# Kernel tuning notes

Hardware: AMD Instinct MI355X
Metric: run time of the kernel (lower is better)

## Reference

```python
import jax, jax.numpy as jnp
import numpy as np

NUM_USERS = 100000
NUM_ITEMS = 50000
EMBED_DIM = 64
NUM_EDGES = 4000000


def setup_inputs() -> dict:
    key = jax.random.key(0)
    k1, k2, k3, k4, k5 = jax.random.split(key, 5)
    u_emb = jax.random.normal(k1, (NUM_USERS, EMBED_DIM), dtype=jnp.float32)
    i_emb = jax.random.normal(k2, (NUM_ITEMS, EMBED_DIM), dtype=jnp.float32)
    user_idx = jax.random.randint(k3, (NUM_EDGES,), 0, 50000, dtype=jnp.int64 if jax.config.jax_enable_x64 else jnp.int32)
    item_idx = jax.random.randint(k4, (NUM_EDGES,), 0, 50000, dtype=jnp.int64 if jax.config.jax_enable_x64 else jnp.int32)
    edge_index = jnp.stack([user_idx, item_idx], axis=0)  # [2, E]
    weights = jax.random.uniform(k5, (NUM_EDGES,), dtype=jnp.float32)
    return {"u_emb": u_emb, "i_emb": i_emb, "edge_index": edge_index, "weights": weights}


def reference(u_emb, i_emb, edge_index, weights):
    user_idx, item_idx = edge_index[0], edge_index[1]
    num_users, num_items = u_emb.shape[0], i_emb.shape[0]
    ones = jnp.ones_like(weights)
    user_deg = jnp.clip(jax.ops.segment_sum(ones, user_idx, num_segments=num_users), 1.0)
    item_deg = jnp.clip(jax.ops.segment_sum(ones, item_idx, num_segments=num_items), 1.0)
    # per-edge symmetric degree normalization: 1/(sqrt(du)*sqrt(di))
    norm = jax.lax.rsqrt(user_deg[user_idx] * item_deg[item_idx])
    edge_w = (weights * norm)[:, None]  # [E, 1]
    new_u_emb = jax.ops.segment_sum(i_emb[item_idx] * edge_w, user_idx, num_segments=num_users)
    new_i_emb = jax.ops.segment_sum(u_emb[user_idx] * edge_w, item_idx, num_segments=num_items)
    return (new_u_emb, new_i_emb)
```

## Files before the change

kernel.cpp:

```cpp
#include <hip/hip_runtime.h>
#include <hip/hip_fp16.h>


#define NUSERS 100000
#define NITEMS 50000
#define EDIM 64
#define NEDGES 4000000

__global__ void degree_kernel(const int* __restrict__ uidx,
                              const int* __restrict__ iidx,
                              int* __restrict__ udeg,
                              int* __restrict__ ideg) {
    int stride = gridDim.x * blockDim.x;
    for (int e = blockIdx.x * blockDim.x + threadIdx.x; e < NEDGES; e += stride) {
        atomicAdd(&udeg[uidx[e]], 1);
        atomicAdd(&ideg[iidx[e]], 1);
    }
}

__global__ void scan_kernel(const int* __restrict__ udeg,
                            const int* __restrict__ ideg,
                            int* __restrict__ u_off, int* __restrict__ i_off,
                            int* __restrict__ u_cur, int* __restrict__ i_cur) {
    __shared__ int partial[1024];
    const int* cnt; int n; int* off; int* cur;
    if (blockIdx.x == 0) { cnt = udeg; n = NUSERS; off = u_off; cur = u_cur; }
    else                 { cnt = ideg; n = NITEMS; off = i_off; cur = i_cur; }

    int tid = threadIdx.x;
    int chunk = (n + 1023) >> 10;
    int s = tid * chunk;
    int e = min(s + chunk, n);

    int sum = 0;
    for (int i = s; i < e; ++i) sum += cnt[i];
    partial[tid] = sum;
    __syncthreads();

    for (int d = 1; d < 1024; d <<= 1) {
        int v = partial[tid];
        int add = (tid >= d) ? partial[tid - d] : 0;
        __syncthreads();
        partial[tid] = v + add;
        __syncthreads();
    }

    int run = partial[tid] - sum;
    for (int i = s; i < e; ++i) {
        off[i] = run;
        cur[i] = run;
        run += cnt[i];
    }
}

__device__ __forceinline__ unsigned pack_rec(int src_idx, float ew) {
    return (unsigned)src_idx |
           ((unsigned)__half_as_ushort(__float2half(ew)) << 16);
}

__global__ void build_u_kernel(const int* __restrict__ uidx,
                               const int* __restrict__ iidx,
                               const float* __restrict__ w,
                               const int* __restrict__ udeg,
                               const int* __restrict__ ideg,
                               int* __restrict__ u_cur,
                               unsigned* __restrict__ u_edges) {
    int stride = gridDim.x * blockDim.x;
    for (int e = blockIdx.x * blockDim.x + threadIdx.x; e < NEDGES; e += stride) {
        int u  = uidx[e];
        int it = iidx[e];
        float ew = w[e] * rsqrtf((float)max(udeg[u], 1) * (float)max(ideg[it], 1));
        int p = atomicAdd(&u_cur[u], 1);
        u_edges[p] = pack_rec(it, ew);
    }
}

__global__ void build_i_kernel(const int* __restrict__ uidx,
                               const int* __restrict__ iidx,
                               const float* __restrict__ w,
                               const int* __restrict__ udeg,
                               const int* __restrict__ ideg,
                               int* __restrict__ i_cur,
                               unsigned* __restrict__ i_edges) {
    int stride = gridDim.x * blockDim.x;
    for (int e = blockIdx.x * blockDim.x + threadIdx.x; e < NEDGES; e += stride) {
        int u  = uidx[e];
        int it = iidx[e];
        float ew = w[e] * rsqrtf((float)max(udeg[u], 1) * (float)max(ideg[it], 1));
        int p = atomicAdd(&i_cur[it], 1);
        i_edges[p] = pack_rec(u, ew);
    }
}

__global__ void gather_kernel(const unsigned* __restrict__ u_edges,
                              const unsigned* __restrict__ i_edges,
                              const int* __restrict__ u_off,
                              const int* __restrict__ i_off,
                              const int* __restrict__ udeg,
                              const int* __restrict__ ideg,
                              const float* __restrict__ u_emb,
                              const float* __restrict__ i_emb,
                              float* __restrict__ out_u,
                              float* __restrict__ out_i) {
    int t = blockIdx.x * blockDim.x + threadIdx.x;
    int row  = t >> 4;
    int lane = t & 15;

    const unsigned* edges; const int* off; const int* deg;
    const float* src; float* out; int r;
    if (row < NUSERS) {
        edges = u_edges; off = u_off; deg = udeg; src = i_emb; out = out_u; r = row;
    } else if (row < NUSERS + NITEMS) {
        edges = i_edges; off = i_off; deg = ideg; src = u_emb; out = out_i; r = row - NUSERS;
    } else {
        return;
    }

    int s = off[r];
    int n = deg[r];
    float4 acc = make_float4(0.f, 0.f, 0.f, 0.f);
    for (int k = 0; k < n; ++k) {
        unsigned rec = edges[s + k];
        float ew = __half2float(__ushort_as_half((unsigned short)(rec >> 16)));
        const float4 v = *reinterpret_cast<const float4*>(
            src + (size_t)(rec & 0xFFFFu) * EDIM + lane * 4);
        acc.x += v.x * ew;
        acc.y += v.y * ew;
        acc.z += v.z * ew;
        acc.w += v.w * ew;
    }
    *reinterpret_cast<float4*>(out + (size_t)r * EDIM + lane * 4) = acc;
}

__global__ void fb_degree_kernel(const int* __restrict__ uidx,
                                 const int* __restrict__ iidx,
                                 float* __restrict__ udeg,
                                 float* __restrict__ ideg) {
    int stride = gridDim.x * blockDim.x;
    for (int e = blockIdx.x * blockDim.x + threadIdx.x; e < NEDGES; e += stride) {
        atomicAdd(&udeg[uidx[e]], 1.0f);
        atomicAdd(&ideg[iidx[e]], 1.0f);
    }
}

__global__ void fb_scatter_kernel(const float* __restrict__ u_emb,
                                  const float* __restrict__ i_emb,
                                  const int* __restrict__ uidx,
                                  const int* __restrict__ iidx,
                                  const float* __restrict__ w,
                                  const float* __restrict__ udeg,
                                  const float* __restrict__ ideg,
                                  float* __restrict__ out_u,
                                  float* __restrict__ out_i) {
    long long t = (long long)blockIdx.x * blockDim.x + threadIdx.x;
    int e    = (int)(t >> 4);
    int lane = (int)(t & 15);
    if (e >= NEDGES) return;
    int u  = uidx[e];
    int it = iidx[e];
    float ew = w[e] * rsqrtf(fmaxf(udeg[u], 1.0f) * fmaxf(ideg[it], 1.0f));
    const float4 iv = *reinterpret_cast<const float4*>(i_emb + (size_t)it * EDIM + lane * 4);
    const float4 uv = *reinterpret_cast<const float4*>(u_emb + (size_t)u  * EDIM + lane * 4);
    float* pu = out_u + (size_t)u  * EDIM + lane * 4;
    float* pi = out_i + (size_t)it * EDIM + lane * 4;
    atomicAdd(pu + 0, iv.x * ew); atomicAdd(pu + 1, iv.y * ew);
    atomicAdd(pu + 2, iv.z * ew); atomicAdd(pu + 3, iv.w * ew);
    atomicAdd(pi + 0, uv.x * ew); atomicAdd(pi + 1, uv.y * ew);
    atomicAdd(pi + 2, uv.z * ew); atomicAdd(pi + 3, uv.w * ew);
}

extern "C" void kernel_launch(void* const* d_in, const int* in_sizes, int n_in,
                              void* d_out, int out_size, void* d_ws, size_t ws_size,
                              hipStream_t stream) {
    const float* u_emb = (const float*)d_in[0];
    const float* i_emb = (const float*)d_in[1];
    const int*   eidx  = (const int*)d_in[2];
    const float* w     = (const float*)d_in[3];

    const int* uidx = eidx;
    const int* iidx = eidx + NEDGES;

    float* out_u = (float*)d_out;
    float* out_i = out_u + (size_t)NUSERS * EDIM;

    size_t need = (size_t)NEDGES * 4 * 2 + (size_t)(NUSERS + NITEMS) * 4 * 3;

    if (ws_size >= need) {
        char* p = (char*)d_ws;
        unsigned* u_edges = (unsigned*)p;          p += (size_t)NEDGES * 4;
        unsigned* i_edges = (unsigned*)p;          p += (size_t)NEDGES * 4;
        int* udeg = (int*)p;                       p += (size_t)NUSERS * 4;
        int* ideg = (int*)p;                       p += (size_t)NITEMS * 4;
        int* u_off = (int*)p;                      p += (size_t)NUSERS * 4;
        int* i_off = (int*)p;                      p += (size_t)NITEMS * 4;
        int* u_cur = (int*)p;                      p += (size_t)NUSERS * 4;
        int* i_cur = (int*)p;

        hipMemsetAsync(udeg, 0, (size_t)(NUSERS + NITEMS) * 4, stream);

        degree_kernel<<<2048, 256, 0, stream>>>(uidx, iidx, udeg, ideg);
        scan_kernel<<<2, 1024, 0, stream>>>(udeg, ideg, u_off, i_off, u_cur, i_cur);
        build_u_kernel<<<2048, 256, 0, stream>>>(uidx, iidx, w, udeg, ideg,
                                                 u_cur, u_edges);
        build_i_kernel<<<2048, 256, 0, stream>>>(uidx, iidx, w, udeg, ideg,
                                                 i_cur, i_edges);
        int rows = NUSERS + NITEMS;
        gather_kernel<<<(rows * 16 + 255) / 256, 256, 0, stream>>>(
            u_edges, i_edges, u_off, i_off, udeg, ideg, u_emb, i_emb, out_u, out_i);
    } else {
        float* udeg = (float*)d_ws;
        float* ideg = udeg + NUSERS;
        hipMemsetAsync(d_ws, 0, (size_t)(NUSERS + NITEMS) * sizeof(float), stream);
        hipMemsetAsync(d_out, 0, (size_t)out_size * sizeof(float), stream);
        fb_degree_kernel<<<2048, 256, 0, stream>>>(uidx, iidx, udeg, ideg);
        long long total_threads = (long long)NEDGES * 16;
        fb_scatter_kernel<<<(int)((total_threads + 255) / 256), 256, 0, stream>>>(
            u_emb, i_emb, uidx, iidx, w, udeg, ideg, out_u, out_i);
    }
}
```

Baseline: 1.310 ms.

## Replicate degree counters and CSR cursors to reduce atomic contention

Degree counting and CSR slot assignment now use NREP=8 replicated counter arrays chosen by block index. A totals kernel sums the replicas for normalization and the scan, and a cursor-init kernel gives each replica its own sub-range within each row's CSR segment. This is meant to spread same-address atomics across copies and cut contention on hot rows. It adds two small kernels, a larger memset and workspace, and needs more workspace, so it may fall back to the atomic scatter path if the buffer is too small.

```diff
diff --git a/kernel.cpp b/kernel.cpp
--- a/kernel.cpp
+++ b/kernel.cpp
@@ -6,26 +6,53 @@
 #define NITEMS 50000
 #define EDIM 64
 #define NEDGES 4000000
-
-__global__ void degree_kernel(const int* __restrict__ uidx,
-                              const int* __restrict__ iidx,
-                              int* __restrict__ udeg,
-                              int* __restrict__ ideg) {
-    int stride = gridDim.x * blockDim.x;
-    for (int e = blockIdx.x * blockDim.x + threadIdx.x; e < NEDGES; e += stride) {
-        atomicAdd(&udeg[uidx[e]], 1);
-        atomicAdd(&ideg[iidx[e]], 1);
-    }
-}
-
-__global__ void scan_kernel(const int* __restrict__ udeg,
-                            const int* __restrict__ ideg,
-                            int* __restrict__ u_off, int* __restrict__ i_off,
-                            int* __restrict__ u_cur, int* __restrict__ i_cur) {
+#define NREP 8
+#define BUILD_GRID 2048
+#define BUILD_BLK 256
+
+__global__ void degree_rep_kernel(const int* __restrict__ uidx,
+                                  const int* __restrict__ iidx,
+                                  int* __restrict__ udeg_rep,
+                                  int* __restrict__ ideg_rep) {
+    int r = blockIdx.x & (NREP - 1);
+    int* __restrict__ ud = udeg_rep + (size_t)r * NUSERS;
+    int* __restrict__ id = ideg_rep + (size_t)r * NITEMS;
+    int stride = gridDim.x * blockDim.x;
+    for (int e = blockIdx.x * blockDim.x + threadIdx.x; e < NEDGES; e += stride) {
+        atomicAdd(&ud[uidx[e]], 1);
+        atomicAdd(&id[iidx[e]], 1);
+    }
+}
+
+__global__ void totals_kernel(const int* __restrict__ udeg_rep,
+                              const int* __restrict__ ideg_rep,
+                              int* __restrict__ udeg_tot,
+                              int* __restrict__ ideg_tot) {
+    int stride = gridDim.x * blockDim.x;
+    for (int row = blockIdx.x * blockDim.x + threadIdx.x;
+         row < NUSERS + NITEMS; row += stride) {
+        if (row < NUSERS) {
+            int s = 0;
+            #pragma unroll
+            for (int r = 0; r < NREP; ++r) s += udeg_rep[(size_t)r * NUSERS + row];
+            udeg_tot[row] = s;
+        } else {
+            int rr = row - NUSERS;
+            int s = 0;
+            #pragma unroll
+            for (int r = 0; r < NREP; ++r) s += ideg_rep[(size_t)r * NITEMS + rr];
+            ideg_tot[rr] = s;
+        }
+    }
+}
+
+__global__ void scan_kernel(const int* __restrict__ udeg_tot,
+                            const int* __restrict__ ideg_tot,
+                            int* __restrict__ u_off, int* __restrict__ i_off) {
     __shared__ int partial[1024];
-    const int* cnt; int n; int* off; int* cur;
-    if (blockIdx.x == 0) { cnt = udeg; n = NUSERS; off = u_off; cur = u_cur; }
-    else                 { cnt = ideg; n = NITEMS; off = i_off; cur = i_cur; }
+    const int* cnt; int n; int* off;
+    if (blockIdx.x == 0) { cnt = udeg_tot; n = NUSERS; off = u_off; }
+    else                 { cnt = ideg_tot; n = NITEMS; off = i_off; }
 
     int tid = threadIdx.x;
     int chunk = (n + 1023) >> 10;
@@ -48,8 +75,35 @@
     int run = partial[tid] - sum;
     for (int i = s; i < e; ++i) {
         off[i] = run;
-        cur[i] = run;
         run += cnt[i];
+    }
+}
+
+__global__ void cur_init_kernel(const int* __restrict__ udeg_rep,
+                                const int* __restrict__ ideg_rep,
+                                const int* __restrict__ u_off,
+                                const int* __restrict__ i_off,
+                                int* __restrict__ u_cur_rep,
+                                int* __restrict__ i_cur_rep) {
+    int stride = gridDim.x * blockDim.x;
+    for (int row = blockIdx.x * blockDim.x + threadIdx.x;
+         row < NUSERS + NITEMS; row += stride) {
+        if (row < NUSERS) {
+            int base = u_off[row];
+            #pragma unroll
+            for (int r = 0; r < NREP; ++r) {
+                u_cur_rep[(size_t)r * NUSERS + row] = base;
+                base += udeg_rep[(size_t)r * NUSERS + row];
+            }
+        } else {
+            int rr = row - NUSERS;
+            int base = i_off[rr];
+            #pragma unroll
+            for (int r = 0; r < NREP; ++r) {
+                i_cur_rep[(size_t)r * NITEMS + rr] = base;
+                base += ideg_rep[(size_t)r * NITEMS + rr];
+            }
+        }
     }
 }
 
@@ -61,16 +115,19 @@
 __global__ void build_u_kernel(const int* __restrict__ uidx,
                                const int* __restrict__ iidx,
                                const float* __restrict__ w,
-                               const int* __restrict__ udeg,
-                               const int* __restrict__ ideg,
-                               int* __restrict__ u_cur,
+                               const int* __restrict__ udeg_tot,
+                               const int* __restrict__ ideg_tot,
+                               int* __restrict__ u_cur_rep,
                                unsigned* __restrict__ u_edges) {
+    int rep = blockIdx.x & (NREP - 1);
+    int* __restrict__ cur = u_cur_rep + (size_t)rep * NUSERS;
     int stride = gridDim.x * blockDim.x;
     for (int e = blockIdx.x * blockDim.x + threadIdx.x; e < NEDGES; e += stride) {
         int u  = uidx[e];
         int it = iidx[e];
-        float ew = w[e] * rsqrtf((float)max(udeg[u], 1) * (float)max(ideg[it], 1));
-        int p = atomicAdd(&u_cur[u], 1);
+        float ew = w[e] * rsqrtf((float)max(udeg_tot[u], 1) *
+                                 (float)max(ideg_tot[it], 1));
+        int p = atomicAdd(&cur[u], 1);
         u_edges[p] = pack_rec(it, ew);
     }
 }
@@ -78,16 +135,19 @@
 __global__ void build_i_kernel(const int* __restrict__ uidx,
                                const int* __restrict__ iidx,
                                const float* __restrict__ w,
-                               const int* __restrict__ udeg,
-                               const int* __restrict__ ideg,
-                               int* __restrict__ i_cur,
+                               const int* __restrict__ udeg_tot,
+                               const int* __restrict__ ideg_tot,
+                               int* __restrict__ i_cur_rep,
                                unsigned* __restrict__ i_edges) {
+    int rep = blockIdx.x & (NREP - 1);
+    int* __restrict__ cur = i_cur_rep + (size_t)rep * NITEMS;
     int stride = gridDim.x * blockDim.x;
     for (int e = blockIdx.x * blockDim.x + threadIdx.x; e < NEDGES; e += stride) {
         int u  = uidx[e];
         int it = iidx[e];
-        float ew = w[e] * rsqrtf((float)max(udeg[u], 1) * (float)max(ideg[it], 1));
-        int p = atomicAdd(&i_cur[it], 1);
+        float ew = w[e] * rsqrtf((float)max(udeg_tot[u], 1) *
+                                 (float)max(ideg_tot[it], 1));
+        int p = atomicAdd(&cur[it], 1);
         i_edges[p] = pack_rec(u, ew);
     }
 }
@@ -96,8 +156,8 @@
                               const unsigned* __restrict__ i_edges,
                               const int* __restrict__ u_off,
                               const int* __restrict__ i_off,
-                              const int* __restrict__ udeg,
-                              const int* __restrict__ ideg,
+                              const int* __restrict__ udeg_tot,
+                              const int* __restrict__ ideg_tot,
                               const float* __restrict__ u_emb,
                               const float* __restrict__ i_emb,
                               float* __restrict__ out_u,
@@ -109,9 +169,10 @@
     const unsigned* edges; const int* off; const int* deg;
     const float* src; float* out; int r;
     if (row < NUSERS) {
-        edges = u_edges; off = u_off; deg = udeg; src = i_emb; out = out_u; r = row;
+        edges = u_edges; off = u_off; deg = udeg_tot; src = i_emb; out = out_u; r = row;
     } else if (row < NUSERS + NITEMS) {
-        edges = i_edges; off = i_off; deg = ideg; src = u_emb; out = out_i; r = row - NUSERS;
+        edges = i_edges; off = i_off; deg = ideg_tot; src = u_emb; out = out_i;
+        r = row - NUSERS;
     } else {
         return;
     }
@@ -183,30 +244,45 @@
     float* out_u = (float*)d_out;
     float* out_i = out_u + (size_t)NUSERS * EDIM;
 
-    size_t need = (size_t)NEDGES * 4 * 2 + (size_t)(NUSERS + NITEMS) * 4 * 3;
+    size_t need = (size_t)NEDGES * 4 * 2
+                + (size_t)(NUSERS + NITEMS) * 4 * (2 * NREP + 2)
+                + (size_t)(NUSERS + NITEMS) * 4;
 
     if (ws_size >= need) {
         char* p = (char*)d_ws;
         unsigned* u_edges = (unsigned*)p;          p += (size_t)NEDGES * 4;
         unsigned* i_edges = (unsigned*)p;          p += (size_t)NEDGES * 4;
-        int* udeg = (int*)p;                       p += (size_t)NUSERS * 4;
-        int* ideg = (int*)p;                       p += (size_t)NITEMS * 4;
+        int* udeg_rep = (int*)p;                   p += (size_t)NREP * NUSERS * 4;
+        int* ideg_rep = (int*)p;                   p += (size_t)NREP * NITEMS * 4;
+        int* udeg_tot = (int*)p;                   p += (size_t)NUSERS * 4;
+        int* ideg_tot = (int*)p;                   p += (size_t)NITEMS * 4;
         int* u_off = (int*)p;                      p += (size_t)NUSERS * 4;
         int* i_off = (int*)p;                      p += (size_t)NITEMS * 4;
-        int* u_cur = (int*)p;                      p += (size_t)NUSERS * 4;
-        int* i_cur = (int*)p;
-
-        hipMemsetAsync(udeg, 0, (size_t)(NUSERS + NITEMS) * 4, stream);
-
-        degree_kernel<<<2048, 256, 0, stream>>>(uidx, iidx, udeg, ideg);
-        scan_kernel<<<2, 1024, 0, stream>>>(udeg, ideg, u_off, i_off, u_cur, i_cur);
-        build_u_kernel<<<2048, 256, 0, stream>>>(uidx, iidx, w, udeg, ideg,
-                                                 u_cur, u_edges);
-        build_i_kernel<<<2048, 256, 0, stream>>>(uidx, iidx, w, udeg, ideg,
-                                                 i_cur, i_edges);
+        int* u_cur_rep = (int*)p;                  p += (size_t)NREP * NUSERS * 4;
+        int* i_cur_rep = (int*)p;
+
+        hipMemsetAsync(udeg_rep, 0, (size_t)NREP * (NUSERS + NITEMS) * 4, stream);
+
+        degree_rep_kernel<<<BUILD_GRID, BUILD_BLK, 0, stream>>>(
+            uidx, iidx, udeg_rep, ideg_rep);
+
         int rows = NUSERS + NITEMS;
+        totals_kernel<<<(rows + 255) / 256, 256, 0, stream>>>(
+            udeg_rep, ideg_rep, udeg_tot, ideg_tot);
+
+        scan_kernel<<<2, 1024, 0, stream>>>(udeg_tot, ideg_tot, u_off, i_off);
+
+        cur_init_kernel<<<(rows + 255) / 256, 256, 0, stream>>>(
+            udeg_rep, ideg_rep, u_off, i_off, u_cur_rep, i_cur_rep);
+
+        build_u_kernel<<<BUILD_GRID, BUILD_BLK, 0, stream>>>(
+            uidx, iidx, w, udeg_tot, ideg_tot, u_cur_rep, u_edges);
+        build_i_kernel<<<BUILD_GRID, BUILD_BLK, 0, stream>>>(
+            uidx, iidx, w, udeg_tot, ideg_tot, i_cur_rep, i_edges);
+
         gather_kernel<<<(rows * 16 + 255) / 256, 256, 0, stream>>>(
-            u_edges, i_edges, u_off, i_off, udeg, ideg, u_emb, i_emb, out_u, out_i);
+            u_edges, i_edges, u_off, i_off, udeg_tot, ideg_tot,
+            u_emb, i_emb, out_u, out_i);
     } else {
         float* udeg = (float*)d_ws;
         float* ideg = udeg + NUSERS;
```

Result: faster. 1.215 ms (-7.2%).
